# Performance work log

Hardware: AMD Instinct MI355X
Metric: run time of the kernel (lower is better)

Reference implementation:

```python
import jax, jax.numpy as jnp
import numpy as np

NUM_TYPES = 200
TOK_DIM = 10000
SMALL_DIM = 64
IN_DIM = 32 + 32 + SMALL_DIM  # 128
NUM_EDGE_TYPES = 3
STEPS = 4
BLOCKS = 2
PROJ_DIM = 128
N_NODES = 100000
N_EDGES = 600000
N_GRAPHS = 64


def setup_inputs() -> dict:
    key = jax.random.key(0)
    ks = jax.random.split(key, 20)
    s = 0.05
    inp = {
        'x_type': jax.random.randint(ks[0], (N_NODES,), 0, NUM_TYPES),
        'x_tok': jax.random.randint(ks[1], (N_NODES,), 0, TOK_DIM + 1),
        'x_small': jax.random.normal(ks[2], (N_NODES, SMALL_DIM), jnp.float32),
        'edge_index': jax.random.randint(ks[3], (2, N_EDGES), 0, N_NODES),
        'edge_type': jax.random.randint(ks[4], (N_EDGES,), 0, NUM_EDGE_TYPES),
        'batch': jnp.sort(jax.random.randint(ks[5], (N_NODES,), 0, N_GRAPHS)),
        # learned params
        'type_emb': jax.random.normal(ks[6], (NUM_TYPES, 32), jnp.float32),
        'tok_emb': jax.random.normal(ks[7], (TOK_DIM + 1, 32), jnp.float32),
        'msg_W': jax.random.normal(ks[8], (NUM_EDGE_TYPES, IN_DIM, IN_DIM), jnp.float32) * s,
        'msg_b': jax.random.normal(ks[9], (NUM_EDGE_TYPES, IN_DIM), jnp.float32) * s,
        'W_ih': jax.random.normal(ks[10], (3 * IN_DIM, IN_DIM), jnp.float32) * s,
        'W_hh': jax.random.normal(ks[11], (3 * IN_DIM, IN_DIM), jnp.float32) * s,
        'b_ih': jax.random.normal(ks[12], (3 * IN_DIM,), jnp.float32) * s,
        'b_hh': jax.random.normal(ks[13], (3 * IN_DIM,), jnp.float32) * s,
        'proj_W1': jax.random.normal(ks[14], (PROJ_DIM, IN_DIM), jnp.float32) * s,
        'proj_b1': jax.random.normal(ks[15], (PROJ_DIM,), jnp.float32) * s,
        'proj_W2': jax.random.normal(ks[16], (1, PROJ_DIM), jnp.float32) * s,
        'proj_b2': jax.random.normal(ks[17], (1,), jnp.float32) * s,
    }
    return inp


def _gru_cell(m, h, W_ih, W_hh, b_ih, b_hh):
    # torch.nn.GRU single step
    gi = m @ W_ih.T + b_ih  # [N, 3H]
    gh = h @ W_hh.T + b_hh
    i_r, i_z, i_n = jnp.split(gi, 3, axis=-1)
    h_r, h_z, h_n = jnp.split(gh, 3, axis=-1)
    r = jax.nn.sigmoid(i_r + h_r)
    z = jax.nn.sigmoid(i_z + h_z)
    n = jnp.tanh(i_n + r * h_n)
    return (1.0 - z) * n + z * h


def reference(x_type, x_tok, x_small, edge_index, edge_type, batch,
              type_emb, tok_emb, msg_W, msg_b,
              W_ih, W_hh, b_ih, b_hh,
              proj_W1, proj_b1, proj_W2, proj_b2):
    n = x_type.shape[0]
    x = jnp.concatenate([type_emb[x_type], tok_emb[x_tok], x_small], axis=-1)  # [N, IN_DIM]
    src, dst = edge_index[0], edge_index[1]
    for _ in range(BLOCKS * STEPS):
        # transform every node once per edge type: [T, N, D]
        h_all = jnp.einsum('ni,toi->tno', x, msg_W) + msg_b[:, None, :]
        # per-edge message = typed linear of source node (gather)
        m = h_all[edge_type, src]  # [E, D]
        agg = jax.ops.segment_sum(m, dst, num_segments=n)  # summed over edge types too
        x = _gru_cell(agg, x, W_ih, W_hh, b_ih, b_hh)
    # global mean pool over graphs
    sums = jax.ops.segment_sum(x, batch, num_segments=N_GRAPHS)
    counts = jax.ops.segment_sum(jnp.ones((n,), x.dtype), batch, num_segments=N_GRAPHS)
    pooled = sums / jnp.maximum(counts, 1.0)[:, None]
    h = jax.nn.relu(pooled @ proj_W1.T + proj_b1)  # dropout = identity in eval
    logits = (h @ proj_W2.T + proj_b2).reshape(-1)
    return logits
```

## Files before the change

kernel.cpp:

```cpp
#include <hip/hip_runtime.h>
#include <stdint.h>


typedef _Float16 f16;
typedef _Float16 v8hf __attribute__((ext_vector_type(8)));
typedef _Float16 v2hf __attribute__((ext_vector_type(2)));
typedef float    v16f __attribute__((ext_vector_type(16)));

#define GI_F 147456
#define GH_F 49152

__device__ __forceinline__ float sigf(float a){
  return __fdividef(1.0f, 1.0f + __expf(-a));
}
__device__ __forceinline__ float tanhf_fast(float a){
  return 1.0f - __fdividef(2.0f, __expf(2.0f*a) + 1.0f);
}

__global__ void k_diag(float* out, int n, float v){
  int i = threadIdx.x; if(i<n) out[i] = v;
}

__global__ void k_embed(const int* __restrict__ xtype, const int* __restrict__ xtok,
                        const float* __restrict__ xsmall,
                        const float* __restrict__ temb, const float* __restrict__ kemb,
                        f16* __restrict__ xb, int N){
  int n = blockIdx.x; int j = threadIdx.x;
  if(n>=N) return;
  float v;
  if(j<32)       v = temb[xtype[n]*32 + j];
  else if(j<64)  v = kemb[xtok[n]*32 + (j-32)];
  else           v = xsmall[(size_t)n*64 + (j-64)];
  xb[(size_t)n*128 + j] = (f16)v;
}

__global__ void k_wcomb(const float* __restrict__ W_ih, const float* __restrict__ msg_W,
                        float* __restrict__ Wc){
  int i = blockIdx.x*256 + threadIdx.x;
  if(i >= 147456) return;
  int o2 = i/384, K = i%384;
  const float* wr = W_ih + o2*128;
  const float* mc = msg_W + (K>>7)*16384 + (K&127);
  float acc = 0.f;
  #pragma unroll 4
  for(int k2=0;k2<128;k2++) acc += wr[k2]*mc[k2*128];
  Wc[i] = acc;
}

__global__ void k_mbp(const float* __restrict__ W_ih, const float* __restrict__ msg_b,
                      float* __restrict__ mbp){
  int i = blockIdx.x*256 + threadIdx.x;
  if(i >= 1152) return;
  int t = i/384, o2 = i%384;
  const float* wr = W_ih + o2*128;
  const float* mb = msg_b + t*128;
  float acc = 0.f;
  #pragma unroll 4
  for(int k2=0;k2<128;k2++) acc += wr[k2]*mb[k2];
  mbp[i] = acc;
}

__global__ void k_wprep(const float* __restrict__ Wc, const float* __restrict__ W_hh,
                        f16* __restrict__ WpF){
  int i = blockIdx.x*256 + threadIdx.x;
  if(i >= GI_F + GH_F) return;
  float w; int lane, j;
  if(i < GI_F){
    int grp = i/512, rem = i%512;
    lane = rem/8; j = rem%8;
    int tile = grp/24, ks = grp%24;
    int n = tile*32 + (lane&31);
    int k = ks*16 + (lane>>5)*8 + j;
    w = Wc[n*384 + k];
  } else {
    int i2 = i - GI_F;
    int grp = i2/512, rem = i2%512;
    lane = rem/8; j = rem%8;
    int tile = grp/8, ks = grp%8;
    int n = tile*32 + (lane&31);
    int k = ks*16 + (lane>>5)*8 + j;
    w = W_hh[n*128 + k];
  }
  WpF[i] = (f16)w;
}

__global__ void k_hist3(const int* __restrict__ dst, const int* __restrict__ et,
                        int* __restrict__ deg3, int E){
  int e = blockIdx.x*blockDim.x + threadIdx.x;
  if(e<E) atomicAdd(&deg3[dst[e]*3 + et[e]], 1);
}

__global__ void k_scan1(const int* __restrict__ deg, int n, int* __restrict__ part, int* __restrict__ bsum){
  __shared__ int s[256];
  int t = threadIdx.x;
  int base = blockIdx.x*1024 + t*4;
  int v[4]; int sum=0;
  #pragma unroll
  for(int k=0;k<4;k++){ int i=base+k; int d=(i<n)?deg[i]:0; sum+=d; v[k]=sum; }
  s[t]=sum; __syncthreads();
  for(int off=1;off<256;off<<=1){
    int add = (t>=off)? s[t-off] : 0;
    __syncthreads();
    s[t]+=add;
    __syncthreads();
  }
  int excl = (t>0)? s[t-1] : 0;
  #pragma unroll
  for(int k=0;k<4;k++){ int i=base+k; if(i<n) part[i]=v[k]+excl; }
  if(t==255) bsum[blockIdx.x] = s[255];
}

__global__ void k_scan2(const int* __restrict__ bsum, int nb, int* __restrict__ carry){
  if(threadIdx.x==0 && blockIdx.x==0){
    int c=0;
    for(int b=0;b<nb;b++){ carry[b]=c; c+=bsum[b]; }
  }
}

__global__ void k_finalize(const int* __restrict__ part, const int* __restrict__ deg,
                           const int* __restrict__ carry, int n,
                           int* __restrict__ rowptr, int* __restrict__ cursor){
  int i = blockIdx.x*blockDim.x + threadIdx.x;
  if(i>=n) return;
  int incl = part[i] + carry[i>>10];
  rowptr[i+1] = incl;
  cursor[i] = incl - deg[i];
  if(i==0) rowptr[0]=0;
}

__global__ void k_fill3(const int* __restrict__ src, const int* __restrict__ dst,
                        const int* __restrict__ et, int* __restrict__ cursor,
                        int* __restrict__ pay, int E){
  int e = blockIdx.x*blockDim.x + threadIdx.x;
  if(e>=E) return;
  int pos = atomicAdd(&cursor[dst[e]*3 + et[e]], 1);
  pay[pos] = src[e];
}

__global__ void k_gather3_b(const f16* __restrict__ xb, const int* __restrict__ rp3,
                            const int* __restrict__ pay, f16* __restrict__ s, int N){
  int n = blockIdx.x*4 + (threadIdx.x>>6);
  if(n >= N) return;
  int lane = threadIdx.x & 63;
  int c = lane*2;
  int b = n*3;
  int i0 = rp3[b],   e0 = rp3[b+1];
  int i1 = e0,       e1 = rp3[b+2];
  int i2 = e1,       e2 = rp3[b+3];
  float a0=0.f,b0=0.f,a1=0.f,b1=0.f,a2=0.f,b2=0.f;
  while(i0<e0 && i1<e1 && i2<e2){
    int p0 = pay[i0], p1 = pay[i1], p2 = pay[i2];
    v2hf u0 = *(const v2hf*)&xb[(size_t)p0*128 + c];
    v2hf u1 = *(const v2hf*)&xb[(size_t)p1*128 + c];
    v2hf u2 = *(const v2hf*)&xb[(size_t)p2*128 + c];
    a0 += (float)u0[0]; b0 += (float)u0[1];
    a1 += (float)u1[0]; b1 += (float)u1[1];
    a2 += (float)u2[0]; b2 += (float)u2[1];
    i0++; i1++; i2++;
  }
  for(; i0<e0; i0++){ v2hf u = *(const v2hf*)&xb[(size_t)pay[i0]*128 + c]; a0+=(float)u[0]; b0+=(float)u[1]; }
  for(; i1<e1; i1++){ v2hf u = *(const v2hf*)&xb[(size_t)pay[i1]*128 + c]; a1+=(float)u[0]; b1+=(float)u[1]; }
  for(; i2<e2; i2++){ v2hf u = *(const v2hf*)&xb[(size_t)pay[i2]*128 + c]; a2+=(float)u[0]; b2+=(float)u[1]; }
  size_t o = (size_t)n*384 + c;
  v2hf t;
  t[0]=(f16)a0; t[1]=(f16)b0; *(v2hf*)&s[o]     = t;
  t[0]=(f16)a1; t[1]=(f16)b1; *(v2hf*)&s[o+128] = t;
  t[0]=(f16)a2; t[1]=(f16)b2; *(v2hf*)&s[o+256] = t;
}

#define SSTR 392
#define XSTR 136
__global__ __launch_bounds__(256,2) void k_mega2(
    const f16* __restrict__ xb_old, f16* __restrict__ xb_new,
    const f16* __restrict__ s, const f16* __restrict__ WpF,
    const int* __restrict__ deg3, const float* __restrict__ mbp,
    const float* __restrict__ b_ih, const float* __restrict__ b_hh, int M)
{
  __shared__ f16 Ss[32*SSTR];
  __shared__ f16 Ax[32*XSTR];
  __shared__ float Dg[96];
  int tid = threadIdx.x, lane = tid & 63, w = tid >> 6;
  int lrow = lane & 31, q = lane >> 5;
  int row0 = blockIdx.x * 32;

  #pragma unroll
  for(int p=0;p<2;p++){
    int ch = tid + p*256;
    int row = ch>>4, c8 = (ch&15)*8;
    int gr = row0 + row; if(gr >= M) gr = M-1;
    *(v8hf*)&Ax[row*XSTR + c8] = *(const v8hf*)(xb_old + (size_t)gr*128 + c8);
  }
  #pragma unroll
  for(int p=0;p<6;p++){
    int ch = tid + p*256;
    int row = ch/48, c8 = (ch%48)*8;
    int gr = row0 + row; if(gr >= M) gr = M-1;
    *(v8hf*)&Ss[row*SSTR + c8] = *(const v8hf*)(s + (size_t)gr*384 + c8);
  }
  if(tid < 96){
    int node = row0 + tid/3;
    Dg[tid] = (node < M) ? (float)deg3[node*3 + (tid - (tid/3)*3)] : 0.f;
  }
  __syncthreads();

  v16f agi[3] = {};
  #pragma unroll
  for(int ks=0; ks<24; ks++){
    int kb = ks*16 + q*8;
    v8hf a0 = *(const v8hf*)&Ss[lrow*SSTR + kb];
    #pragma unroll
    for(int ct=0; ct<3; ct++){
      int tile = ct*4 + w;
      v8hf bh = *(const v8hf*)(WpF + (size_t)(tile*24 + ks)*512 + lane*8);
      agi[ct] = __builtin_amdgcn_mfma_f32_32x32x16_f16(a0, bh, agi[ct], 0,0,0);
    }
  }
  v2hf gip[3][8];
  #pragma unroll
  for(int ct=0; ct<3; ct++)
    #pragma unroll
    for(int rp=0; rp<8; rp++){
      v2hf t; t[0] = (f16)agi[ct][2*rp]; t[1] = (f16)agi[ct][2*rp+1];
      gip[ct][rp] = t;
    }

  v16f agh[3] = {};
  #pragma unroll
  for(int ks=0; ks<8; ks++){
    int kb = ks*16 + q*8;
    v8hf a0 = *(const v8hf*)&Ax[lrow*XSTR + kb];
    #pragma unroll
    for(int ct=0; ct<3; ct++){
      int tile = ct*4 + w;
      v8hf bh = *(const v8hf*)(WpF + GI_F + (size_t)(tile*8 + ks)*512 + lane*8);
      agh[ct] = __builtin_amdgcn_mfma_f32_32x32x16_f16(a0, bh, agh[ct], 0,0,0);
    }
  }

  int jf = w*32 + lrow;
  float bi0 = b_ih[jf],     bh0 = b_hh[jf];
  float bi1 = b_ih[128+jf], bh1 = b_hh[128+jf];
  float bi2 = b_ih[256+jf], bh2 = b_hh[256+jf];
  float mb[3][3];
  #pragma unroll
  for(int t=0;t<3;t++){
    mb[t][0] = mbp[t*384 + jf];
    mb[t][1] = mbp[t*384 + 128 + jf];
    mb[t][2] = mbp[t*384 + 256 + jf];
  }
  int rq4 = 4*q;
  #pragma unroll
  for(int r=0;r<16;r++){
    int gl = (r&3) + 8*(r>>2) + rq4;
    float d0 = Dg[gl*3], d1 = Dg[gl*3+1], d2 = Dg[gl*3+2];
    float g0 = (float)gip[0][r>>1][r&1];
    float g1 = (float)gip[1][r>>1][r&1];
    float g2 = (float)gip[2][r>>1][r&1];
    float ir  = g0 + bi0 + d0*mb[0][0] + d1*mb[1][0] + d2*mb[2][0];
    float iz  = g1 + bi1 + d0*mb[0][1] + d1*mb[1][1] + d2*mb[2][1];
    float in_ = g2 + bi2 + d0*mb[0][2] + d1*mb[1][2] + d2*mb[2][2];
    float hr  = agh[0][r] + bh0;
    float hz  = agh[1][r] + bh1;
    float hn  = agh[2][r] + bh2;
    float rg = sigf(ir + hr);
    float zg = sigf(iz + hz);
    float nn = tanhf_fast(in_ + rg*hn);
    float xo = (float)Ax[gl*XSTR + jf];
    Ax[gl*XSTR + jf] = (f16)((1.f - zg)*nn + zg*xo);
  }
  __syncthreads();
  #pragma unroll
  for(int p=0;p<2;p++){
    int ch = tid + p*256;
    int row = ch>>4, c8 = (ch&15)*8;
    int gr = row0 + row;
    if(gr < M)
      *(v8hf*)(xb_new + (size_t)gr*128 + c8) = *(const v8hf*)&Ax[row*XSTR + c8];
  }
}

__device__ __forceinline__ int lb_batch(const int* __restrict__ batch, int N, int g){
  int lo=0, hi=N;
  while(lo<hi){ int mid=(lo+hi)>>1; if(batch[mid]<g) lo=mid+1; else hi=mid; }
  return lo;
}

__global__ void k_pool2(const f16* __restrict__ xb, const int* __restrict__ batch,
                        float* __restrict__ pooled, int N){
  int g = blockIdx.x, slice = blockIdx.y;
  int j = threadIdx.x;
  int lo = lb_batch(batch,N,g), hi = lb_batch(batch,N,g+1);
  float acc = 0.f;
  for(int r=lo+slice; r<hi; r+=32) acc += (float)xb[(size_t)r*128 + j];
  atomicAdd(&pooled[g*128+j], acc);
}

__global__ void k_head(const float* __restrict__ pooled, const int* __restrict__ batch, int N,
                       const float* __restrict__ W1, const float* __restrict__ b1,
                       const float* __restrict__ W2, const float* __restrict__ b2,
                       float* __restrict__ out){
  int g = blockIdx.x; int j = threadIdx.x;
  __shared__ float p[128];
  __shared__ float red[128];
  int lo = lb_batch(batch,N,g), hi = lb_batch(batch,N,g+1);
  float c = (float)(hi-lo); if(c < 1.f) c = 1.f;
  p[j] = pooled[g*128+j] / c;
  __syncthreads();
  float acc = b1[j];
  #pragma unroll 4
  for(int i=0;i<128;i++) acc += W1[j*128+i]*p[i];
  float v = (acc>0.f?acc:0.f) * W2[j];
  red[j] = v; __syncthreads();
  for(int s=64;s>0;s>>=1){ if(j<s) red[j]+=red[j+s]; __syncthreads(); }
  if(j==0) out[g] = red[0] + b2[0];
}

extern "C" void kernel_launch(void* const* d_in, const int* in_sizes, int n_in,
                              void* d_out, int out_size, void* d_ws, size_t ws_size,
                              hipStream_t stream){
  const int*   x_type    = (const int*)d_in[0];
  const int*   x_tok     = (const int*)d_in[1];
  const float* x_small   = (const float*)d_in[2];
  const int*   edge_index= (const int*)d_in[3];
  const int*   edge_type = (const int*)d_in[4];
  const int*   batch     = (const int*)d_in[5];
  const float* type_emb  = (const float*)d_in[6];
  const float* tok_emb   = (const float*)d_in[7];
  const float* msg_W     = (const float*)d_in[8];
  const float* msg_b     = (const float*)d_in[9];
  const float* W_ih      = (const float*)d_in[10];
  const float* W_hh      = (const float*)d_in[11];
  const float* b_ih      = (const float*)d_in[12];
  const float* b_hh      = (const float*)d_in[13];
  const float* pW1       = (const float*)d_in[14];
  const float* pb1       = (const float*)d_in[15];
  const float* pW2       = (const float*)d_in[16];
  const float* pb2       = (const float*)d_in[17];
  float* out = (float*)d_out;

  int N = in_sizes[0];
  int E = in_sizes[3]/2;
  const int* src = edge_index;
  const int* dst = edge_index + E;
  int n3 = 3*N;
  int nch = (n3+1023)/1024;

  char* w = (char*)d_ws;
  size_t off = 0;
  auto alloc = [&](size_t bytes)->char*{ char* p = w + off; off += (bytes + 511) & ~511ull; return p; };
  f16*   xb0    = (f16*)alloc((size_t)N*128*2);
  f16*   xb1    = (f16*)alloc((size_t)N*128*2);
  f16*   s      = (f16*)alloc((size_t)N*384*2);
  int*   deg3   = (int*)alloc((size_t)n3*4);
  int*   part   = (int*)alloc((size_t)n3*4);
  int*   rp3    = (int*)alloc((size_t)(n3+1)*4);
  int*   cursor = (int*)alloc((size_t)n3*4);
  int*   pay    = (int*)alloc((size_t)E*4);
  int*   bsum   = (int*)alloc((size_t)nch*4);
  int*   carry  = (int*)alloc((size_t)nch*4);
  float* Wc     = (float*)alloc((size_t)147456*4);
  f16*   WpF    = (f16*)alloc((size_t)(GI_F+GH_F)*2);
  float* mbp    = (float*)alloc((size_t)1152*4);
  float* pooled = (float*)alloc(64*128*4);
  if(off > ws_size){
    k_diag<<<1,64,0,stream>>>(out, out_size, 1.0e6f + (float)(ws_size>>20));
    return;
  }

  const int tb = 256;
  hipMemsetAsync(deg3, 0, (size_t)n3*4, stream);
  k_wcomb   <<<576, 256, 0, stream>>>(W_ih, msg_W, Wc);
  k_mbp     <<<5, 256, 0, stream>>>(W_ih, msg_b, mbp);
  k_wprep   <<<(GI_F+GH_F+255)/256, 256, 0, stream>>>(Wc, W_hh, WpF);
  k_hist3   <<<(E+tb-1)/tb, tb, 0, stream>>>(dst, edge_type, deg3, E);
  k_scan1   <<<nch, 256, 0, stream>>>(deg3, n3, part, bsum);
  k_scan2   <<<1, 64, 0, stream>>>(bsum, nch, carry);
  k_finalize<<<(n3+tb-1)/tb, tb, 0, stream>>>(part, deg3, carry, n3, rp3, cursor);
  k_fill3   <<<(E+tb-1)/tb, tb, 0, stream>>>(src, dst, edge_type, cursor, pay, E);
  k_embed   <<<N, 128, 0, stream>>>(x_type, x_tok, x_small, type_emb, tok_emb, xb0, N);

  int nblk = (N+31)/32;
  f16* xin = xb0;
  f16* xout = xb1;
  for(int it=0; it<8; it++){
    k_gather3_b<<<(N+3)/4, 256, 0, stream>>>(xin, rp3, pay, s, N);
    k_mega2    <<<nblk, 256, 0, stream>>>(xin, xout, s, WpF, deg3, mbp, b_ih, b_hh, N);
    f16* tmp = xin; xin = xout; xout = tmp;
  }
  hipMemsetAsync(pooled, 0, 64*128*4, stream);
  k_pool2<<<dim3(64,32), 128, 0, stream>>>(xin, batch, pooled, N);
  k_head <<<64, 128, 0, stream>>>(pooled, batch, N, pW1, pb1, pW2, pb2, out);
}
```

Baseline: 1.282 ms.

## Process 64 rows per block in fused GRU kernel, splitting K into two halves

The fused message/GRU kernel now handles 64 node rows per workgroup instead of 32. Each weight fragment loaded from global memory feeds two MFMA row tiles, halving weight traffic per row. To keep shared memory bounded, the 384-wide aggregated input is staged in two 192-column halves with extra barriers between them. This doubles accumulator registers (12 v16f accumulators plus the packed gi values), which may spill or cut occupancy below the two blocks per CU requested in the launch bounds, and it halves the number of workgroups.

```diff
diff --git a/kernel.cpp b/kernel.cpp
--- a/kernel.cpp
+++ b/kernel.cpp
@@ -168,7 +168,7 @@
   t[0]=(f16)a2; t[1]=(f16)b2; *(v2hf*)&s[o+256] = t;
 }
 
-#define SSTR 392
+#define SSTR2 200
 #define XSTR 136
 __global__ __launch_bounds__(256,2) void k_mega2(
     const f16* __restrict__ xb_old, f16* __restrict__ xb_new,
@@ -176,15 +176,15 @@
     const int* __restrict__ deg3, const float* __restrict__ mbp,
     const float* __restrict__ b_ih, const float* __restrict__ b_hh, int M)
 {
-  __shared__ f16 Ss[32*SSTR];
-  __shared__ f16 Ax[32*XSTR];
-  __shared__ float Dg[96];
+  __shared__ f16 Ss[64*SSTR2];
+  __shared__ f16 Ax[64*XSTR];
+  __shared__ float Dg[192];
   int tid = threadIdx.x, lane = tid & 63, w = tid >> 6;
   int lrow = lane & 31, q = lane >> 5;
-  int row0 = blockIdx.x * 32;
-
-  #pragma unroll
-  for(int p=0;p<2;p++){
+  int row0 = blockIdx.x * 64;
+
+  #pragma unroll
+  for(int p=0;p<4;p++){
     int ch = tid + p*256;
     int row = ch>>4, c8 = (ch&15)*8;
     int gr = row0 + row; if(gr >= M) gr = M-1;
@@ -193,49 +193,79 @@
   #pragma unroll
   for(int p=0;p<6;p++){
     int ch = tid + p*256;
-    int row = ch/48, c8 = (ch%48)*8;
+    int row = ch/24, c8 = (ch%24)*8;
     int gr = row0 + row; if(gr >= M) gr = M-1;
-    *(v8hf*)&Ss[row*SSTR + c8] = *(const v8hf*)(s + (size_t)gr*384 + c8);
-  }
-  if(tid < 96){
+    *(v8hf*)&Ss[row*SSTR2 + c8] = *(const v8hf*)(s + (size_t)gr*384 + c8);
+  }
+  if(tid < 192){
     int node = row0 + tid/3;
     Dg[tid] = (node < M) ? (float)deg3[node*3 + (tid - (tid/3)*3)] : 0.f;
   }
   __syncthreads();
 
-  v16f agi[3] = {};
-  #pragma unroll
-  for(int ks=0; ks<24; ks++){
+  v16f agi[2][3] = {};
+  #pragma unroll
+  for(int ks=0; ks<12; ks++){
     int kb = ks*16 + q*8;
-    v8hf a0 = *(const v8hf*)&Ss[lrow*SSTR + kb];
+    v8hf a0 = *(const v8hf*)&Ss[(     lrow)*SSTR2 + kb];
+    v8hf a1 = *(const v8hf*)&Ss[(32 + lrow)*SSTR2 + kb];
     #pragma unroll
     for(int ct=0; ct<3; ct++){
       int tile = ct*4 + w;
       v8hf bh = *(const v8hf*)(WpF + (size_t)(tile*24 + ks)*512 + lane*8);
-      agi[ct] = __builtin_amdgcn_mfma_f32_32x32x16_f16(a0, bh, agi[ct], 0,0,0);
+      agi[0][ct] = __builtin_amdgcn_mfma_f32_32x32x16_f16(a0, bh, agi[0][ct], 0,0,0);
+      agi[1][ct] = __builtin_amdgcn_mfma_f32_32x32x16_f16(a1, bh, agi[1][ct], 0,0,0);
     }
   }
-  v2hf gip[3][8];
-  #pragma unroll
-  for(int ct=0; ct<3; ct++)
+  __syncthreads();
+  #pragma unroll
+  for(int p=0;p<6;p++){
+    int ch = tid + p*256;
+    int row = ch/24, c8 = (ch%24)*8;
+    int gr = row0 + row; if(gr >= M) gr = M-1;
+    *(v8hf*)&Ss[row*SSTR2 + c8] = *(const v8hf*)(s + (size_t)gr*384 + 192 + c8);
+  }
+  __syncthreads();
+  #pragma unroll
+  for(int ks2=0; ks2<12; ks2++){
+    int ks = ks2 + 12;
+    int kb = ks2*16 + q*8;
+    v8hf a0 = *(const v8hf*)&Ss[(     lrow)*SSTR2 + kb];
+    v8hf a1 = *(const v8hf*)&Ss[(32 + lrow)*SSTR2 + kb];
     #pragma unroll
-    for(int rp=0; rp<8; rp++){
-      v2hf t; t[0] = (f16)agi[ct][2*rp]; t[1] = (f16)agi[ct][2*rp+1];
-      gip[ct][rp] = t;
+    for(int ct=0; ct<3; ct++){
+      int tile = ct*4 + w;
+      v8hf bh = *(const v8hf*)(WpF + (size_t)(tile*24 + ks)*512 + lane*8);
+      agi[0][ct] = __builtin_amdgcn_mfma_f32_32x32x16_f16(a0, bh, agi[0][ct], 0,0,0);
+      agi[1][ct] = __builtin_amdgcn_mfma_f32_32x32x16_f16(a1, bh, agi[1][ct], 0,0,0);
     }
-
-  v16f agh[3] = {};
+  }
+  v2hf gip[2][3][8];
+  #pragma unroll
+  for(int rt=0; rt<2; rt++)
+    #pragma unroll
+    for(int ct=0; ct<3; ct++)
+      #pragma unroll
+      for(int rp=0; rp<8; rp++){
+        v2hf t; t[0] = (f16)agi[rt][ct][2*rp]; t[1] = (f16)agi[rt][ct][2*rp+1];
+        gip[rt][ct][rp] = t;
+      }
+
+  v16f agh[2][3] = {};
   #pragma unroll
   for(int ks=0; ks<8; ks++){
     int kb = ks*16 + q*8;
-    v8hf a0 = *(const v8hf*)&Ax[lrow*XSTR + kb];
+    v8hf a0 = *(const v8hf*)&Ax[(     lrow)*XSTR + kb];
+    v8hf a1 = *(const v8hf*)&Ax[(32 + lrow)*XSTR + kb];
     #pragma unroll
     for(int ct=0; ct<3; ct++){
       int tile = ct*4 + w;
       v8hf bh = *(const v8hf*)(WpF + GI_F + (size_t)(tile*8 + ks)*512 + lane*8);
-      agh[ct] = __builtin_amdgcn_mfma_f32_32x32x16_f16(a0, bh, agh[ct], 0,0,0);
+      agh[0][ct] = __builtin_amdgcn_mfma_f32_32x32x16_f16(a0, bh, agh[0][ct], 0,0,0);
+      agh[1][ct] = __builtin_amdgcn_mfma_f32_32x32x16_f16(a1, bh, agh[1][ct], 0,0,0);
     }
   }
+  __syncthreads();
 
   int jf = w*32 + lrow;
   float bi0 = b_ih[jf],     bh0 = b_hh[jf];
@@ -250,27 +280,30 @@
   }
   int rq4 = 4*q;
   #pragma unroll
-  for(int r=0;r<16;r++){
-    int gl = (r&3) + 8*(r>>2) + rq4;
-    float d0 = Dg[gl*3], d1 = Dg[gl*3+1], d2 = Dg[gl*3+2];
-    float g0 = (float)gip[0][r>>1][r&1];
-    float g1 = (float)gip[1][r>>1][r&1];
-    float g2 = (float)gip[2][r>>1][r&1];
-    float ir  = g0 + bi0 + d0*mb[0][0] + d1*mb[1][0] + d2*mb[2][0];
-    float iz  = g1 + bi1 + d0*mb[0][1] + d1*mb[1][1] + d2*mb[2][1];
-    float in_ = g2 + bi2 + d0*mb[0][2] + d1*mb[1][2] + d2*mb[2][2];
-    float hr  = agh[0][r] + bh0;
-    float hz  = agh[1][r] + bh1;
-    float hn  = agh[2][r] + bh2;
-    float rg = sigf(ir + hr);
-    float zg = sigf(iz + hz);
-    float nn = tanhf_fast(in_ + rg*hn);
-    float xo = (float)Ax[gl*XSTR + jf];
-    Ax[gl*XSTR + jf] = (f16)((1.f - zg)*nn + zg*xo);
-  }
-  __syncthreads();
-  #pragma unroll
-  for(int p=0;p<2;p++){
+  for(int rt=0; rt<2; rt++){
+    #pragma unroll
+    for(int r=0;r<16;r++){
+      int gl = rt*32 + (r&3) + 8*(r>>2) + rq4;
+      float d0 = Dg[gl*3], d1 = Dg[gl*3+1], d2 = Dg[gl*3+2];
+      float g0 = (float)gip[rt][0][r>>1][r&1];
+      float g1 = (float)gip[rt][1][r>>1][r&1];
+      float g2 = (float)gip[rt][2][r>>1][r&1];
+      float ir  = g0 + bi0 + d0*mb[0][0] + d1*mb[1][0] + d2*mb[2][0];
+      float iz  = g1 + bi1 + d0*mb[0][1] + d1*mb[1][1] + d2*mb[2][1];
+      float in_ = g2 + bi2 + d0*mb[0][2] + d1*mb[1][2] + d2*mb[2][2];
+      float hr  = agh[rt][0][r] + bh0;
+      float hz  = agh[rt][1][r] + bh1;
+      float hn  = agh[rt][2][r] + bh2;
+      float rg = sigf(ir + hr);
+      float zg = sigf(iz + hz);
+      float nn = tanhf_fast(in_ + rg*hn);
+      float xo = (float)Ax[gl*XSTR + jf];
+      Ax[gl*XSTR + jf] = (f16)((1.f - zg)*nn + zg*xo);
+    }
+  }
+  __syncthreads();
+  #pragma unroll
+  for(int p=0;p<4;p++){
     int ch = tid + p*256;
     int row = ch>>4, c8 = (ch&15)*8;
     int gr = row0 + row;
@@ -379,7 +412,7 @@
   k_fill3   <<<(E+tb-1)/tb, tb, 0, stream>>>(src, dst, edge_type, cursor, pay, E);
   k_embed   <<<N, 128, 0, stream>>>(x_type, x_tok, x_small, type_emb, tok_emb, xb0, N);
 
-  int nblk = (N+31)/32;
+  int nblk = (N+63)/64;
   f16* xin = xb0;
   f16* xout = xb1;
   for(int it=0; it<8; it++){
```

New measurement: 1.756 ms. 1.37x slower.
